# Kernel optimization log

Measured on AMD Instinct MI355X. Metric: run time of the kernel, lower is better.

## Reference

```python
import jax, jax.numpy as jnp
import numpy as np

N_NODES = 100000
N_EDGES = 1600000
IN_C = 128
OUT_C = 64
NEG_SLOPE = 0.2  # PyG GATConv default
EPS = 1e-16      # PyG softmax denominator guard


def setup_inputs() -> dict:
    key = jax.random.key(0)
    k1, k2, k3, k4, k5, k6 = jax.random.split(key, 6)
    x = jax.random.normal(k1, (N_NODES, IN_C), dtype=jnp.float32)
    edge_index = jax.random.randint(k2, (2, N_EDGES), 0, N_NODES, dtype=jnp.int64)
    # Learned params (GATConv with heads=1): linear weight, attention vectors, bias
    W = jax.random.normal(k3, (IN_C, OUT_C), dtype=jnp.float32) * (1.0 / np.sqrt(IN_C))
    a_src = jax.random.normal(k4, (OUT_C,), dtype=jnp.float32) * (1.0 / np.sqrt(OUT_C))
    a_dst = jax.random.normal(k5, (OUT_C,), dtype=jnp.float32) * (1.0 / np.sqrt(OUT_C))
    b = jax.random.normal(k6, (OUT_C,), dtype=jnp.float32) * 0.01
    return {"x": x, "edge_index": edge_index, "W": W, "a_src": a_src, "a_dst": a_dst, "b": b}


def reference(x, edge_index, W, a_src, a_dst, b):
    N = x.shape[0]
    h = x @ W  # [N, OUT_C] transformed node features
    # add self loops (PyG default add_self_loops=True)
    loops = jnp.arange(N, dtype=edge_index.dtype)
    src = jnp.concatenate([edge_index[0], loops])  # [E+N]
    dst = jnp.concatenate([edge_index[1], loops])  # [E+N]
    # attention logits per edge: leaky_relu(a_src . h_src + a_dst . h_dst)
    s_src = h @ a_src  # [N]
    s_dst = h @ a_dst  # [N]
    logits = jax.nn.leaky_relu(s_src[src] + s_dst[dst], NEG_SLOPE)  # [E+N]
    # segment softmax over incoming edges of each destination node
    seg_max = jax.ops.segment_max(logits, dst, num_segments=N)  # [N]
    e = jnp.exp(logits - seg_max[dst])
    denom = jax.ops.segment_sum(e, dst, num_segments=N)  # [N]
    coef = e / (denom[dst] + EPS)  # [E+N]
    # weighted scatter-add of source messages
    out = jax.ops.segment_sum(coef[:, None] * h[src], dst, num_segments=N) + b  # [N, OUT_C]
    return jax.nn.elu(out)
```

## Files before the change

kernel.cpp:

```cpp
#include <hip/hip_runtime.h>
#include <math.h>

#define IN_C 128
#define OUT_C 64
#define NEG_SLOPE 0.2f
#define GAT_EPS 1e-16f

#define FSH 6
#define FN 64
#define CAPB 1536
#define PACKS 20
#define CHUNK 8192
#define NFBA 1568
#define CSTR 4

typedef unsigned int uint;
typedef unsigned short ushort;
typedef __attribute__((ext_vector_type(8))) short bf16x8;
typedef __attribute__((ext_vector_type(4))) float f32x4;

__device__ __forceinline__ ushort f2bf(float f) {
    uint u = __float_as_uint(f);
    return (ushort)((u + 0x7fffu + ((u >> 16) & 1u)) >> 16);
}

__global__ __launch_bounds__(256) void gemm_kernel(
    const float* __restrict__ x, const float* __restrict__ W,
    const float* __restrict__ a_src, const float* __restrict__ a_dst,
    ushort* __restrict__ h16, float* __restrict__ s_src, float* __restrict__ s_dst,
    int N, int* __restrict__ zero_ptr, int zero_n)
{
    __shared__ __align__(16) ushort xs[64 * 128];
    __shared__ __align__(16) ushort Wl[128 * 64];
    const int t = threadIdx.x;

    {
        int zi = blockIdx.x * 256 + t;
        if (zi < zero_n) zero_ptr[zi] = 0;
    }

    #pragma unroll
    for (int q = 0; q < 8; q++) {
        float4 wv = ((const float4*)W)[t * 8 + q];
        #pragma unroll
        for (int e = 0; e < 4; e++) {
            int L = t * 32 + q * 4 + e;
            int k = L >> 6, col = L & 63;
            int kc = k >> 5, kg = (k >> 3) & 3, j = k & 7;
            int ct = col >> 4, c16 = col & 15;
            float v = (e == 0) ? wv.x : (e == 1) ? wv.y : (e == 2) ? wv.z : wv.w;
            Wl[(((kc * 4 + ct) * 4 + kg) * 16 + c16) * 8 + j] = f2bf(v);
        }
    }
    const int row0 = blockIdx.x * 64;
    {
        int row_l = t >> 2;
        int grow = row0 + row_l;
        #pragma unroll
        for (int qq = 0; qq < 4; qq++) {
            int kq = (t & 3) * 4 + qq;
            float4 v0 = make_float4(0.f, 0.f, 0.f, 0.f);
            float4 v1 = v0;
            if (grow < N) {
                const float4* xp = (const float4*)(x + (size_t)grow * IN_C + kq * 8);
                v0 = xp[0]; v1 = xp[1];
            }
            uint4 pk;
            pk.x = (uint)f2bf(v0.x) | ((uint)f2bf(v0.y) << 16);
            pk.y = (uint)f2bf(v0.z) | ((uint)f2bf(v0.w) << 16);
            pk.z = (uint)f2bf(v1.x) | ((uint)f2bf(v1.y) << 16);
            pk.w = (uint)f2bf(v1.z) | ((uint)f2bf(v1.w) << 16);
            int slot = row_l * 16 + (kq ^ (row_l & 7));
            *(uint4*)&xs[slot * 8] = pk;
        }
    }
    __syncthreads();

    const int wv_ = t >> 6;
    const int l = t & 63;
    const int c16 = l & 15;
    const int quad = l >> 4;
    const int row_a = wv_ * 16 + c16;

    f32x4 acc[4] = {{0.f, 0.f, 0.f, 0.f}, {0.f, 0.f, 0.f, 0.f},
                    {0.f, 0.f, 0.f, 0.f}, {0.f, 0.f, 0.f, 0.f}};

    #pragma unroll
    for (int kc = 0; kc < 4; kc++) {
        int kq = kc * 4 + quad;
        bf16x8 a = *(const bf16x8*)&xs[(row_a * 16 + (kq ^ (row_a & 7))) * 8];
        #pragma unroll
        for (int ct = 0; ct < 4; ct++) {
            bf16x8 b = *(const bf16x8*)&Wl[(((kc * 4 + ct) * 4 + quad) * 16 + c16) * 8];
            acc[ct] = __builtin_amdgcn_mfma_f32_16x16x32_bf16(a, b, acc[ct], 0, 0, 0);
        }
    }

    float as4[4], ad4[4];
    #pragma unroll
    for (int ct = 0; ct < 4; ct++) {
        as4[ct] = a_src[ct * 16 + c16];
        ad4[ct] = a_dst[ct * 16 + c16];
    }
    #pragma unroll
    for (int reg = 0; reg < 4; reg++) {
        int row = row0 + wv_ * 16 + quad * 4 + reg;
        float ps = acc[0][reg] * as4[0] + acc[1][reg] * as4[1]
                 + acc[2][reg] * as4[2] + acc[3][reg] * as4[3];
        float pd = acc[0][reg] * ad4[0] + acc[1][reg] * ad4[1]
                 + acc[2][reg] * ad4[2] + acc[3][reg] * ad4[3];
        ps += __shfl_xor(ps, 1);  pd += __shfl_xor(pd, 1);
        ps += __shfl_xor(ps, 2);  pd += __shfl_xor(pd, 2);
        ps += __shfl_xor(ps, 4);  pd += __shfl_xor(pd, 4);
        ps += __shfl_xor(ps, 8);  pd += __shfl_xor(pd, 8);
        if (row < N) {
            #pragma unroll
            for (int ct = 0; ct < 4; ct++)
                h16[(size_t)row * OUT_C + ct * 16 + c16] = f2bf(acc[ct][reg]);
            if (c16 == 0) { s_src[row] = ps; s_dst[row] = pd; }
        }
    }
}

__global__ __launch_bounds__(256) void bin2_kernel(
    const int* __restrict__ src, const int* __restrict__ dst,
    int* __restrict__ ccur, int* __restrict__ ebufB, int E)
{
    __shared__ int hist[NFBA];
    __shared__ int bcur[NFBA];
    const int t = threadIdx.x;
    const int e0 = blockIdx.x * CHUNK;
    int tot = E - e0; if (tot > CHUNK) tot = CHUNK;

    for (int i = t; i < NFBA; i += 256) hist[i] = 0;
    __syncthreads();
    for (int i = t; i < tot; i += 256)
        atomicAdd(&hist[dst[e0 + i] >> FSH], 1);
    __syncthreads();
    for (int fb = t; fb < NFBA; fb += 256) {
        int v = hist[fb];
        bcur[fb] = (v > 0) ? atomicAdd(&ccur[fb * CSTR], v) : 0;
    }
    __syncthreads();
    for (int i = t; i < tot; i += 256) {
        int dd = dst[e0 + i];
        int ss = src[e0 + i];
        int fb = dd >> FSH;
        int pos = atomicAdd(&bcur[fb], 1);
        if (pos < CAPB)
            ebufB[(size_t)fb * CAPB + pos] = ((dd & (FN - 1)) << PACKS) | ss;
    }
}

__global__ __launch_bounds__(256) void nodeB_kernel(
    const int* __restrict__ ccurB, const int* __restrict__ ebufB,
    const float* __restrict__ s_src, const float* __restrict__ s_dst,
    const ushort* __restrict__ h16, const float* __restrict__ bias,
    float* __restrict__ out, int N)
{
    __shared__ int   csr_s[CAPB];
    __shared__ float csr_e[CAPB];
    __shared__ int lhist[FN], lofs[FN + 1], lcur[FN];

    const int b = blockIdx.x;
    const int t = threadIdx.x;
    const int node0 = b << FSH;
    const int nn = min(FN, N - node0);
    int cnt = ccurB[b * CSTR]; if (cnt > CAPB) cnt = CAPB;
    const int base = b * CAPB;

    if (t < FN) lhist[t] = 0;
    __syncthreads();
    for (int i = t; i < cnt; i += 256)
        atomicAdd(&lhist[(ebufB[base + i] >> PACKS) & (FN - 1)], 1);
    __syncthreads();
    if (t < FN) {
        int v = lhist[t];
        int incl = v;
        #pragma unroll
        for (int off = 1; off < FN; off <<= 1) {
            int u = __shfl_up(incl, off);
            if (t >= off) incl += u;
        }
        lofs[t + 1] = incl;
        lcur[t] = incl - v;
        if (t == 0) lofs[0] = 0;
    }
    __syncthreads();
    for (int i = t; i < cnt; i += 256) {
        int pk = ebufB[base + i];
        int ld = (pk >> PACKS) & (FN - 1);
        int sj = pk & ((1 << PACKS) - 1);
        int q = atomicAdd(&lcur[ld], 1);
        float lg = s_src[sj] + s_dst[node0 + ld];
        lg = (lg > 0.f) ? lg : NEG_SLOPE * lg;
        csr_s[q] = sj;
        csr_e[q] = __expf(lg);
    }
    __syncthreads();

    const int w = t >> 6;
    const int l = t & 63;
    const int h2 = l >> 5;
    const int lp = l & 31;
    const float b0 = bias[2 * lp], b1 = bias[2 * lp + 1];

    for (int nl = w; nl < nn; nl += 4) {
        const int node = node0 + nl;
        const int jb = lofs[nl], je = lofs[nl + 1];
        float acc0 = 0.f, acc1 = 0.f, ds = 0.f;
        int j = jb + h2;
        for (; j + 6 < je; j += 8) {
            int s0 = csr_s[j],     s1 = csr_s[j + 2];
            int s2 = csr_s[j + 4], s3 = csr_s[j + 6];
            float e0 = csr_e[j],     e1 = csr_e[j + 2];
            float e2 = csr_e[j + 4], e3 = csr_e[j + 6];
            uint u0 = *(const uint*)&h16[(size_t)s0 * OUT_C + 2 * lp];
            uint u1 = *(const uint*)&h16[(size_t)s1 * OUT_C + 2 * lp];
            uint u2 = *(const uint*)&h16[(size_t)s2 * OUT_C + 2 * lp];
            uint u3 = *(const uint*)&h16[(size_t)s3 * OUT_C + 2 * lp];
            ds += (e0 + e1) + (e2 + e3);
            acc0 += e0 * __uint_as_float(u0 << 16) + e1 * __uint_as_float(u1 << 16)
                  + e2 * __uint_as_float(u2 << 16) + e3 * __uint_as_float(u3 << 16);
            acc1 += e0 * __uint_as_float(u0 & 0xffff0000u) + e1 * __uint_as_float(u1 & 0xffff0000u)
                  + e2 * __uint_as_float(u2 & 0xffff0000u) + e3 * __uint_as_float(u3 & 0xffff0000u);
        }
        for (; j < je; j += 2) {
            int sj = csr_s[j];
            float e = csr_e[j];
            uint u = *(const uint*)&h16[(size_t)sj * OUT_C + 2 * lp];
            ds += e;
            acc0 += e * __uint_as_float(u << 16);
            acc1 += e * __uint_as_float(u & 0xffff0000u);
        }
        acc0 += __shfl_xor(acc0, 32);
        acc1 += __shfl_xor(acc1, 32);
        ds   += __shfl_xor(ds, 32);

        float ls = s_src[node] + s_dst[node];
        ls = (ls > 0.f) ? ls : NEG_SLOPE * ls;
        float es = __expf(ls);
        uint us = *(const uint*)&h16[(size_t)node * OUT_C + 2 * lp];
        acc0 += es * __uint_as_float(us << 16);
        acc1 += es * __uint_as_float(us & 0xffff0000u);
        ds += es;

        float inv = 1.f / (ds + GAT_EPS);
        float v0 = acc0 * inv + b0;
        float v1 = acc1 * inv + b1;
        v0 = (v0 > 0.f) ? v0 : (__expf(v0) - 1.f);
        v1 = (v1 > 0.f) ? v1 : (__expf(v1) - 1.f);
        if (l < 32) *(float2*)&out[(size_t)node * OUT_C + 2 * lp] = make_float2(v0, v1);
    }
}

extern "C" void kernel_launch(void* const* d_in, const int* in_sizes, int n_in,
                              void* d_out, int out_size, void* d_ws, size_t ws_size,
                              hipStream_t stream)
{
    const float* x     = (const float*)d_in[0];
    const int*   ei    = (const int*)d_in[1];
    const float* W     = (const float*)d_in[2];
    const float* a_src = (const float*)d_in[3];
    const float* a_dst = (const float*)d_in[4];
    const float* b     = (const float*)d_in[5];
    float* out = (float*)d_out;

    const int N = in_sizes[0] / IN_C;
    const int E = in_sizes[1] / 2;
    const int NFB = (N + FN - 1) >> FSH;
    const int GB = (N + 63) / 64;
    const int GBIN = (E + CHUNK - 1) / CHUNK;
    const int* src = ei;
    const int* dst = ei + E;

    ushort* h16    = (ushort*)d_ws;
    float* s_src_p = (float*)(h16 + (size_t)N * OUT_C);
    float* s_dst_p = s_src_p + N;
    int*   ccur    = (int*)(s_dst_p + N);
    int*   ebufB   = ccur + NFBA * CSTR;

    gemm_kernel<<<GB, 256, 0, stream>>>(x, W, a_src, a_dst, h16, s_src_p, s_dst_p,
                                        N, ccur, NFBA * CSTR);
    bin2_kernel<<<GBIN, 256, 0, stream>>>(src, dst, ccur, ebufB, E);
    nodeB_kernel<<<NFB, 256, 0, stream>>>(ccur, ebufB, s_src_p, s_dst_p, h16, b, out, N);
}
```

Before: 208.4 us.

## Fuse GEMM and edge binning into one heterogeneous launch

Merges the feature GEMM and the edge-binning pass into a single kernel where the first blocks bin edges and the rest run the GEMM, so the two independent stages overlap on the GPU. The counter zeroing moves to a separate small kernel, since binning blocks can no longer rely on the GEMM launch having cleared the counters. The binning path now uses vectorized int4 loads, caches packed edges in shared memory to avoid re-reading src, and halves the chunk size to get more binning blocks. Shared memory is unioned into one 32KB buffer, and the extra launch adds some fixed overhead.

Result: faster. 193.5 us (-7.1%).

```diff
diff --git a/kernel.cpp b/kernel.cpp
--- a/kernel.cpp
+++ b/kernel.cpp
@@ -10,9 +10,10 @@
 #define FN 64
 #define CAPB 1536
 #define PACKS 20
-#define CHUNK 8192
+#define CHUNK 4096
 #define NFBA 1568
 #define CSTR 4
+#define SMEM_BYTES 32768
 
 typedef unsigned int uint;
 typedef unsigned short ushort;
@@ -24,20 +25,94 @@
     return (ushort)((u + 0x7fffu + ((u >> 16) & 1u)) >> 16);
 }
 
-__global__ __launch_bounds__(256) void gemm_kernel(
+__global__ __launch_bounds__(256) void zero_kernel(int* __restrict__ p, int n)
+{
+    int i = blockIdx.x * 256 + threadIdx.x;
+    if (i < n) p[i] = 0;
+}
+
+__global__ __launch_bounds__(256) void fusedAB_kernel(
     const float* __restrict__ x, const float* __restrict__ W,
     const float* __restrict__ a_src, const float* __restrict__ a_dst,
     ushort* __restrict__ h16, float* __restrict__ s_src, float* __restrict__ s_dst,
-    int N, int* __restrict__ zero_ptr, int zero_n)
+    int N, const int* __restrict__ src, const int* __restrict__ dst,
+    int* __restrict__ ccur, int* __restrict__ ebufB, int E, int gbin)
 {
-    __shared__ __align__(16) ushort xs[64 * 128];
-    __shared__ __align__(16) ushort Wl[128 * 64];
+    __shared__ __align__(16) char smem[SMEM_BYTES];
     const int t = threadIdx.x;
 
-    {
-        int zi = blockIdx.x * 256 + t;
-        if (zi < zero_n) zero_ptr[zi] = 0;
-    }
+    if ((int)blockIdx.x < gbin) {
+        int* hist = (int*)smem;
+        int* bcur = (int*)(smem + 6272);
+        int* rbuf = (int*)(smem + 12544);
+        const int e0 = blockIdx.x * CHUNK;
+        int tot = E - e0; if (tot > CHUNK) tot = CHUNK;
+
+        for (int i = t; i < NFBA; i += 256) hist[i] = 0;
+        __syncthreads();
+
+        const int i0 = t * 16;
+        #pragma unroll
+        for (int q4 = 0; q4 < 4; q4++) {
+            int ib = i0 + q4 * 4;
+            if (ib + 3 < tot) {
+                int4 d4 = *(const int4*)(dst + e0 + ib);
+                int4 s4 = *(const int4*)(src + e0 + ib);
+                int dd_[4] = {d4.x, d4.y, d4.z, d4.w};
+                int ss_[4] = {s4.x, s4.y, s4.z, s4.w};
+                #pragma unroll
+                for (int k = 0; k < 4; k++) {
+                    atomicAdd(&hist[dd_[k] >> FSH], 1);
+                    rbuf[ib + k] = ((dd_[k] & (FN - 1)) << PACKS) | ss_[k];
+                }
+            } else {
+                for (int k = 0; k < 4; k++) {
+                    int i = ib + k;
+                    if (i < tot) {
+                        int dd = dst[e0 + i], ss = src[e0 + i];
+                        atomicAdd(&hist[dd >> FSH], 1);
+                        rbuf[i] = ((dd & (FN - 1)) << PACKS) | ss;
+                    }
+                }
+            }
+        }
+        __syncthreads();
+
+        for (int fb = t; fb < NFBA; fb += 256) {
+            int v = hist[fb];
+            bcur[fb] = (v > 0) ? atomicAdd(&ccur[fb * CSTR], v) : 0;
+        }
+        __syncthreads();
+
+        #pragma unroll
+        for (int q4 = 0; q4 < 4; q4++) {
+            int ib = i0 + q4 * 4;
+            if (ib + 3 < tot) {
+                int4 d4 = *(const int4*)(dst + e0 + ib);
+                int fb_[4] = {d4.x >> FSH, d4.y >> FSH, d4.z >> FSH, d4.w >> FSH};
+                #pragma unroll
+                for (int k = 0; k < 4; k++) {
+                    int pos = atomicAdd(&bcur[fb_[k]], 1);
+                    if (pos < CAPB)
+                        ebufB[(size_t)fb_[k] * CAPB + pos] = rbuf[ib + k];
+                }
+            } else {
+                for (int k = 0; k < 4; k++) {
+                    int i = ib + k;
+                    if (i < tot) {
+                        int fb = dst[e0 + i] >> FSH;
+                        int pos = atomicAdd(&bcur[fb], 1);
+                        if (pos < CAPB)
+                            ebufB[(size_t)fb * CAPB + pos] = rbuf[i];
+                    }
+                }
+            }
+        }
+        return;
+    }
+
+    ushort* xs = (ushort*)smem;
+    ushort* Wl = (ushort*)(smem + 16384);
 
     #pragma unroll
     for (int q = 0; q < 8; q++) {
@@ -52,7 +127,7 @@
             Wl[(((kc * 4 + ct) * 4 + kg) * 16 + c16) * 8 + j] = f2bf(v);
         }
     }
-    const int row0 = blockIdx.x * 64;
+    const int row0 = (blockIdx.x - gbin) * 64;
     {
         int row_l = t >> 2;
         int grow = row0 + row_l;
@@ -119,36 +194,6 @@
                 h16[(size_t)row * OUT_C + ct * 16 + c16] = f2bf(acc[ct][reg]);
             if (c16 == 0) { s_src[row] = ps; s_dst[row] = pd; }
         }
-    }
-}
-
-__global__ __launch_bounds__(256) void bin2_kernel(
-    const int* __restrict__ src, const int* __restrict__ dst,
-    int* __restrict__ ccur, int* __restrict__ ebufB, int E)
-{
-    __shared__ int hist[NFBA];
-    __shared__ int bcur[NFBA];
-    const int t = threadIdx.x;
-    const int e0 = blockIdx.x * CHUNK;
-    int tot = E - e0; if (tot > CHUNK) tot = CHUNK;
-
-    for (int i = t; i < NFBA; i += 256) hist[i] = 0;
-    __syncthreads();
-    for (int i = t; i < tot; i += 256)
-        atomicAdd(&hist[dst[e0 + i] >> FSH], 1);
-    __syncthreads();
-    for (int fb = t; fb < NFBA; fb += 256) {
-        int v = hist[fb];
-        bcur[fb] = (v > 0) ? atomicAdd(&ccur[fb * CSTR], v) : 0;
-    }
-    __syncthreads();
-    for (int i = t; i < tot; i += 256) {
-        int dd = dst[e0 + i];
-        int ss = src[e0 + i];
-        int fb = dd >> FSH;
-        int pos = atomicAdd(&bcur[fb], 1);
-        if (pos < CAPB)
-            ebufB[(size_t)fb * CAPB + pos] = ((dd & (FN - 1)) << PACKS) | ss;
     }
 }
 
@@ -271,6 +316,7 @@
     const int NFB = (N + FN - 1) >> FSH;
     const int GB = (N + 63) / 64;
     const int GBIN = (E + CHUNK - 1) / CHUNK;
+    const int NZ = NFBA * CSTR;
     const int* src = ei;
     const int* dst = ei + E;
 
@@ -278,10 +324,11 @@
     float* s_src_p = (float*)(h16 + (size_t)N * OUT_C);
     float* s_dst_p = s_src_p + N;
     int*   ccur    = (int*)(s_dst_p + N);
-    int*   ebufB   = ccur + NFBA * CSTR;
-
-    gemm_kernel<<<GB, 256, 0, stream>>>(x, W, a_src, a_dst, h16, s_src_p, s_dst_p,
-                                        N, ccur, NFBA * CSTR);
-    bin2_kernel<<<GBIN, 256, 0, stream>>>(src, dst, ccur, ebufB, E);
+    int*   ebufB   = ccur + NZ;
+
+    zero_kernel<<<(NZ + 255) / 256, 256, 0, stream>>>(ccur, NZ);
+    fusedAB_kernel<<<GBIN + GB, 256, 0, stream>>>(x, W, a_src, a_dst, h16,
+                                                  s_src_p, s_dst_p, N,
+                                                  src, dst, ccur, ebufB, E, GBIN);
     nodeB_kernel<<<NFB, 256, 0, stream>>>(ccur, ebufB, s_src_p, s_dst_p, h16, b, out, N);
 }
```
